# Kernel optimization log

Measured on AMD Instinct MI355X. Metric: run time of the kernel, lower is better.

The kernel has to match this reference:

```python
import jax, jax.numpy as jnp
import numpy as np

N_GRAPHS = 64

def setup_inputs() -> dict:
    key = jax.random.key(0)
    ks = jax.random.split(key, 8)
    N, E, H = 50000, 600000, 128
    x = jax.random.normal(ks[0], (N, 2), dtype=jnp.float32)
    edge_index = jax.random.randint(ks[1], (2, E), 0, N, dtype=jnp.int64)
    batch = jnp.sort(jax.random.randint(ks[2], (N,), 0, N_GRAPHS, dtype=jnp.int64))
    s = 0.1  # keep tanh out of saturation
    return {
        'x': x,
        'edge_index': edge_index,
        'batch': batch,
        'W1': jax.random.normal(ks[3], (2, H), dtype=jnp.float32) * s,
        'b1': jnp.zeros((H,), jnp.float32),
        'W2': jax.random.normal(ks[4], (H, H), dtype=jnp.float32) * s,
        'b2': jnp.zeros((H,), jnp.float32),
        'W3': jax.random.normal(ks[5], (H, H), dtype=jnp.float32) * s,
        'b3': jnp.zeros((H,), jnp.float32),
        'Wo': jax.random.normal(ks[6], (2 * H, 41), dtype=jnp.float32) * s,
        'bo': jnp.zeros((41,), jnp.float32),
    }

def reference(x, edge_index, batch, W1, b1, W2, b2, W3, b3, Wo, bo):
    N = x.shape[0]
    src, dst = edge_index[0], edge_index[1]
    # GCN symmetric normalization with self loops: deg = in-degree + 1
    ones_e = jnp.ones(src.shape[0], dtype=x.dtype)
    deg = jax.ops.segment_sum(ones_e, dst, num_segments=N) + 1.0
    dinv = jax.lax.rsqrt(deg)                       # [N]
    edge_norm = (dinv[src] * dinv[dst])[:, None]    # [E,1]
    self_norm = (dinv * dinv)[:, None]              # [N,1]

    def gcn(h, W, b):
        h = h @ W                                   # [N,H] transform first
        agg = jax.ops.segment_sum(h[src] * edge_norm, dst, num_segments=N)
        return agg + h * self_norm + b

    h = jnp.tanh(gcn(x, W1, b1))
    h = jnp.tanh(gcn(h, W2, b2))
    h = jnp.tanh(gcn(h, W3, b3))

    # global max pool + global mean pool over graphs
    cnt = jax.ops.segment_sum(jnp.ones(N, dtype=h.dtype), batch, num_segments=N_GRAPHS)
    mx = jax.ops.segment_max(h, batch, num_segments=N_GRAPHS)
    mx = jnp.where(cnt[:, None] > 0, mx, 0.0)
    mean = jax.ops.segment_sum(h, batch, num_segments=N_GRAPHS) / jnp.maximum(cnt, 1.0)[:, None]
    pooled = jnp.concatenate([mx, mean], axis=1)    # [G, 2H]
    return jnp.tanh(pooled @ Wo + bo)               # [G, 41]
```

## Files before the change

### kernel.cpp

```cpp
#include <hip/hip_runtime.h>
#include <math.h>

#define NGRAPH 64
#define SCAN_BLK 1024
#define COLCAP 6144
#define AXCAP 2560

typedef short short8 __attribute__((ext_vector_type(8)));
typedef float floatx4 __attribute__((ext_vector_type(4)));

__device__ inline unsigned pack_bf16x2(float a, float b) {
    unsigned ua = __float_as_uint(a);
    unsigned ub = __float_as_uint(b);
    ua = (ua + 0x7fffu + ((ua >> 16) & 1u)) >> 16;
    ub = (ub + 0x7fffu + ((ub >> 16) & 1u)) >> 16;
    return ua | (ub << 16);
}
__device__ inline float bf16lo(unsigned u) { return __uint_as_float(u << 16); }
__device__ inline float bf16hi(unsigned u) { return __uint_as_float(u & 0xffff0000u); }

__device__ inline float ftanh(float x) {
    float cx = fminf(fmaxf(x, -9.f), 9.f);
    float e = __expf(2.f * cx);
    return (e - 1.f) * __frcp_rn(e + 1.f);
}

__device__ inline unsigned fkey(float v) {
    unsigned u = __float_as_uint(v);
    return (v >= 0.f) ? (u | 0x80000000u) : ~u;
}


#define TIDX(u) ((size_t)((qb + (unsigned)(u)) * 4u + (unsigned)q))
#define ACC4() do {                                                       \
    uint4 v0 = t4[TIDX(u0)]; uint4 v1 = t4[TIDX(u1)];                     \
    uint4 v2 = t4[TIDX(u2)]; uint4 v3 = t4[TIDX(u3)];                     \
    a[0] += bf16lo(v0.x); a[1] += bf16hi(v0.x);                           \
    a[2] += bf16lo(v0.y); a[3] += bf16hi(v0.y);                           \
    a[4] += bf16lo(v0.z); a[5] += bf16hi(v0.z);                           \
    a[6] += bf16lo(v0.w); a[7] += bf16hi(v0.w);                           \
    a[0] += bf16lo(v1.x); a[1] += bf16hi(v1.x);                           \
    a[2] += bf16lo(v1.y); a[3] += bf16hi(v1.y);                           \
    a[4] += bf16lo(v1.z); a[5] += bf16hi(v1.z);                           \
    a[6] += bf16lo(v1.w); a[7] += bf16hi(v1.w);                           \
    a[0] += bf16lo(v2.x); a[1] += bf16hi(v2.x);                           \
    a[2] += bf16lo(v2.y); a[3] += bf16hi(v2.y);                           \
    a[4] += bf16lo(v2.z); a[5] += bf16hi(v2.z);                           \
    a[6] += bf16lo(v2.w); a[7] += bf16hi(v2.w);                           \
    a[0] += bf16lo(v3.x); a[1] += bf16hi(v3.x);                           \
    a[2] += bf16lo(v3.y); a[3] += bf16hi(v3.y);                           \
    a[4] += bf16lo(v3.z); a[5] += bf16hi(v3.z);                           \
    a[6] += bf16lo(v3.w); a[7] += bf16hi(v3.w);                           \
} while (0)
#define ACC4M() do {                                                      \
    uint4 v0 = t4[TIDX(u0)]; uint4 v1 = t4[TIDX(u1)];                     \
    uint4 v2 = t4[TIDX(u2)]; uint4 v3 = t4[TIDX(u3)];                     \
    a[0] += bf16lo(v0.x); a[1] += bf16hi(v0.x);                           \
    a[2] += bf16lo(v0.y); a[3] += bf16hi(v0.y);                           \
    a[4] += bf16lo(v0.z); a[5] += bf16hi(v0.z);                           \
    a[6] += bf16lo(v0.w); a[7] += bf16hi(v0.w);                           \
    a[0] = fmaf(m1, bf16lo(v1.x), a[0]); a[1] = fmaf(m1, bf16hi(v1.x), a[1]); \
    a[2] = fmaf(m1, bf16lo(v1.y), a[2]); a[3] = fmaf(m1, bf16hi(v1.y), a[3]); \
    a[4] = fmaf(m1, bf16lo(v1.z), a[4]); a[5] = fmaf(m1, bf16hi(v1.z), a[5]); \
    a[6] = fmaf(m1, bf16lo(v1.w), a[6]); a[7] = fmaf(m1, bf16hi(v1.w), a[7]); \
    a[0] = fmaf(m2, bf16lo(v2.x), a[0]); a[1] = fmaf(m2, bf16hi(v2.x), a[1]); \
    a[2] = fmaf(m2, bf16lo(v2.y), a[2]); a[3] = fmaf(m2, bf16hi(v2.y), a[3]); \
    a[4] = fmaf(m2, bf16lo(v2.z), a[4]); a[5] = fmaf(m2, bf16hi(v2.z), a[5]); \
    a[6] = fmaf(m2, bf16lo(v2.w), a[6]); a[7] = fmaf(m2, bf16hi(v2.w), a[7]); \
    a[0] = fmaf(m3, bf16lo(v3.x), a[0]); a[1] = fmaf(m3, bf16hi(v3.x), a[1]); \
    a[2] = fmaf(m3, bf16lo(v3.y), a[2]); a[3] = fmaf(m3, bf16hi(v3.y), a[3]); \
    a[4] = fmaf(m3, bf16lo(v3.z), a[4]); a[5] = fmaf(m3, bf16hi(v3.z), a[5]); \
    a[6] = fmaf(m3, bf16lo(v3.w), a[6]); a[7] = fmaf(m3, bf16hi(v3.w), a[7]); \
} while (0)


__global__ void pack_count(const int* __restrict__ dst, int E, int* __restrict__ cnt,
                           int* __restrict__ rank,
                           const float* __restrict__ W2, const float* __restrict__ W3,
                           unsigned* __restrict__ Wt2, unsigned* __restrict__ Wt3) {
    if (blockIdx.x < 32) {
        int b = blockIdx.x;
        const float* W = (b < 16) ? W2 : W3;
        unsigned* Wt = (b < 16) ? Wt2 : Wt3;
        b &= 15;
        int bk = b & 3, bn = b >> 2;
        __shared__ float s[32][33];
        int tx = threadIdx.x & 31, ty = threadIdx.x >> 5;
#pragma unroll
        for (int r = 0; r < 4; ++r)
            s[r * 8 + ty][tx] = W[(bk * 32 + r * 8 + ty) * 128 + bn * 32 + tx];
        __syncthreads();
        int t16 = threadIdx.x & 15, tn = threadIdx.x >> 4;
#pragma unroll
        for (int pass = 0; pass < 2; ++pass) {
            int nl = pass * 16 + tn;
            unsigned pk = pack_bf16x2(s[2 * t16][nl], s[2 * t16 + 1][nl]);
            Wt[(bn * 32 + nl) * 64 + bk * 16 + t16] = pk;
        }
    } else {
        int e = (blockIdx.x - 32) * blockDim.x + threadIdx.x;
        if (e < E) rank[e] = atomicAdd(&cnt[dst[e]], 1);
    }
}


__global__ __launch_bounds__(SCAN_BLK) void scanA(const int* __restrict__ cnt,
                                                  const float* __restrict__ x,
                                                  int* __restrict__ row_ptr,
                                                  int* __restrict__ bsum,
                                                  float* __restrict__ dinv,
                                                  float2* __restrict__ y,
                                                  const int* __restrict__ batch,
                                                  int* __restrict__ ticket,
                                                  int* __restrict__ goff, int N) {
    __shared__ int sm[SCAN_BLK];
    __shared__ int amLast;
    int i = blockIdx.x * SCAN_BLK + threadIdx.x;
    int v = (i < N) ? cnt[i] : 0;
    if (i < N) {
        float dv = rsqrtf((float)v + 1.0f);
        dinv[i] = dv;
        float2 xv = ((const float2*)x)[i];
        y[i] = make_float2(xv.x * dv, xv.y * dv);
    }
    sm[threadIdx.x] = v;
    __syncthreads();
    for (int off = 1; off < SCAN_BLK; off <<= 1) {
        int t = (threadIdx.x >= (unsigned)off) ? sm[threadIdx.x - off] : 0;
        __syncthreads();
        sm[threadIdx.x] += t;
        __syncthreads();
    }
    if (i < N) row_ptr[i] = sm[threadIdx.x] - v;
    if (threadIdx.x == SCAN_BLK - 1) bsum[blockIdx.x] = sm[SCAN_BLK - 1];
    __syncthreads();
    if (threadIdx.x == 0) {
        __threadfence();
        amLast = (atomicAdd(ticket, 1) == (int)gridDim.x - 1);
    }
    __syncthreads();
    if (!amLast) return;
    int nb = (int)gridDim.x;
    int v2 = (threadIdx.x < (unsigned)nb) ? atomicAdd(&bsum[threadIdx.x], 0) : 0;
    sm[threadIdx.x] = v2;
    __syncthreads();
    for (int off = 1; off < SCAN_BLK; off <<= 1) {
        int t = (threadIdx.x >= (unsigned)off) ? sm[threadIdx.x - off] : 0;
        __syncthreads();
        sm[threadIdx.x] += t;
        __syncthreads();
    }
    if (threadIdx.x < (unsigned)nb) bsum[threadIdx.x] = sm[threadIdx.x] - v2;
    if (threadIdx.x <= NGRAPH) {
        int g = threadIdx.x;
        int lo = 0, hi = N;
        while (lo < hi) {
            int mid = (lo + hi) >> 1;
            if (batch[mid] < g) lo = mid + 1; else hi = mid;
        }
        goff[g] = lo;
    }
}

__global__ void fill_kernel(const int* __restrict__ src, const int* __restrict__ dst, int E,
                            const int* __restrict__ row_ptr, const int* __restrict__ bsum,
                            const int* __restrict__ rank, int* __restrict__ col) {
    int e = blockIdx.x * blockDim.x + threadIdx.x;
    if (e < E) {
        int d = dst[e];
        int p = row_ptr[d] + bsum[d >> 10] + rank[e];
        col[p] = src[e];
    }
}


__global__ __launch_bounds__(256) void agg_x_t1(const float2* __restrict__ y,
                                                const int* __restrict__ row_ptr,
                                                const int* __restrict__ bsum,
                                                const int* __restrict__ col,
                                                const float* __restrict__ dinv,
                                                const float* __restrict__ W1,
                                                const float* __restrict__ b1,
                                                unsigned short* __restrict__ h, int N, int E) {
    __shared__ float4 sW[64];
    __shared__ float4 sb[32];
    __shared__ float2 zs[64];
    __shared__ int scol[AXCAP];
    if (threadIdx.x < 64) sW[threadIdx.x] = ((const float4*)W1)[threadIdx.x];
    if (threadIdx.x >= 64 && threadIdx.x < 96) sb[threadIdx.x - 64] = ((const float4*)b1)[threadIdx.x - 64];

    int firstNode = blockIdx.x * 64;
    int lastNode = min(firstNode + 64, N);
    int sBase = row_ptr[firstNode] + bsum[firstNode >> 10];
    int eEnd = (lastNode < N) ? row_ptr[lastNode] + bsum[lastNode >> 10] : E;
    int range = eEnd - sBase;
    bool inLds = (range <= AXCAP);
    if (inLds) {
        for (int i = threadIdx.x; i < range; i += 256) scol[i] = col[sBase + i];
    }
    __syncthreads();

    int grp = threadIdx.x >> 2;
    int l4 = threadIdx.x & 3;
    int node = firstNode + grp;
    float ax = 0.f, ay = 0.f;
    if (node < N) {
        int s = row_ptr[node] + bsum[node >> 10];
        int e = (node + 1 < N) ? row_ptr[node + 1] + bsum[(node + 1) >> 10] : E;
        int deg = e - s;
        if (inLds) {
            int sl = s - sBase;
            int j = l4;
            for (; j + 4 < deg; j += 8) {
                float2 v0 = y[scol[sl + j]];
                float2 v1 = y[scol[sl + j + 4]];
                ax += v0.x; ay += v0.y;
                ax += v1.x; ay += v1.y;
            }
            if (j < deg) { float2 v = y[scol[sl + j]]; ax += v.x; ay += v.y; }
        } else {
            int j = l4;
            for (; j + 4 < deg; j += 8) {
                float2 v0 = y[col[s + j]];
                float2 v1 = y[col[s + j + 4]];
                ax += v0.x; ay += v0.y;
                ax += v1.x; ay += v1.y;
            }
            if (j < deg) { float2 v = y[col[s + j]]; ax += v.x; ay += v.y; }
        }
    }
    ax += __shfl_xor(ax, 1, 64); ay += __shfl_xor(ay, 1, 64);
    ax += __shfl_xor(ax, 2, 64); ay += __shfl_xor(ay, 2, 64);
    if (l4 == 0 && node < N) {
        float2 self = y[node];
        float dv = dinv[node];
        zs[grp] = make_float2(dv * (ax + self.x), dv * (ay + self.y));
    }
    __syncthreads();

    int q = threadIdx.x & 31;
    int rsub = threadIdx.x >> 5;
    float4 w0 = sW[q];
    float4 w1 = sW[32 + q];
    float4 b = sb[q];
    size_t qoff = (size_t)(q >> 3) * N;
#pragma unroll
    for (int pass = 0; pass < 8; ++pass) {
        int local = pass * 8 + rsub;
        int row = firstNode + local;
        if (row >= N) break;
        float2 z = zs[local];
        float ox = ftanh(fmaf(z.x, w0.x, fmaf(z.y, w1.x, b.x)));
        float oy = ftanh(fmaf(z.x, w0.y, fmaf(z.y, w1.y, b.y)));
        float oz = ftanh(fmaf(z.x, w0.z, fmaf(z.y, w1.z, b.z)));
        float ow = ftanh(fmaf(z.x, w0.w, fmaf(z.y, w1.w, b.w)));
        uint2 pk;
        pk.x = pack_bf16x2(ox, oy);
        pk.y = pack_bf16x2(oz, ow);
        ((uint2*)h)[(qoff + row) * 8 + (q & 7)] = pk;
    }
}


__global__ __launch_bounds__(256) void gemm_mfma(const unsigned short* __restrict__ A,
                                                 const unsigned* __restrict__ Wt,
                                                 const float* __restrict__ dinv,
                                                 unsigned short* __restrict__ t, int N) {
    __shared__ unsigned sW[128 * 68];
    const uint4* Wt4 = (const uint4*)Wt;
    for (int i = threadIdx.x; i < 2048; i += 256) {
        int n = i >> 4, c = i & 15;
        *(uint4*)&sW[n * 68 + c * 4] = Wt4[i];
    }
    __syncthreads();
    int l = threadIdx.x & 63;
    int w = threadIdx.x >> 6;
    int lm = l & 15;
    int q4 = l >> 4;

    floatx4 acc[2][8];
#pragma unroll
    for (int i = 0; i < 2; ++i)
#pragma unroll
        for (int j = 0; j < 8; ++j) acc[i][j] = (floatx4){0.f, 0.f, 0.f, 0.f};

    int rowbase = blockIdx.x * 128 + w * 32;
    int k8 = q4 * 8;
#pragma unroll
    for (int ks = 0; ks < 4; ++ks) {
        short8 a[2];
#pragma unroll
        for (int mt = 0; mt < 2; ++mt) {
            int r = min(rowbase + mt * 16 + lm, N - 1);
            a[mt] = *(const short8*)(A + ((size_t)ks * N + r) * 32 + k8);
        }
#pragma unroll
        for (int nt = 0; nt < 8; ++nt) {
            short8 b = *(const short8*)&sW[(nt * 16 + lm) * 68 + ks * 16 + q4 * 4];
#pragma unroll
            for (int mt = 0; mt < 2; ++mt)
                acc[mt][nt] = __builtin_amdgcn_mfma_f32_16x16x32_bf16(b, a[mt], acc[mt][nt], 0, 0, 0);
        }
    }

#pragma unroll
    for (int mt = 0; mt < 2; ++mt) {
        int gr = rowbase + mt * 16 + lm;
        if (gr < N) {
            float dv = dinv[gr];
#pragma unroll
            for (int nt = 0; nt < 8; ++nt) {
                uint2 pk;
                pk.x = pack_bf16x2(acc[mt][nt][0] * dv, acc[mt][nt][1] * dv);
                pk.y = pack_bf16x2(acc[mt][nt][2] * dv, acc[mt][nt][3] * dv);
                *(uint2*)(t + ((size_t)(nt >> 1) * N + gr) * 32 + (nt & 1) * 16 + q4 * 4) = pk;
            }
        }
    }
}


__global__ __launch_bounds__(1024) void agg_kernel(const unsigned short* __restrict__ t,
                                                   const int* __restrict__ row_ptr,
                                                   const int* __restrict__ bsum,
                                                   const int* __restrict__ col,
                                                   const float* __restrict__ dinv,
                                                   const float* __restrict__ bias,
                                                   unsigned short* __restrict__ out, int N, int E) {
    int nchunk = (N + 255) >> 8;
    int bid = (int)blockIdx.x;
    int r8 = bid & 7;
    int qt = r8 >> 1;
    int c = (bid >> 3) * 2 + (r8 & 1);
    if (c >= nchunk) return;

    __shared__ int scol[COLCAP];
    int firstNode = c * 256;
    int lastNode = min(firstNode + 256, N);
    int sBase = row_ptr[firstNode] + bsum[firstNode >> 10];
    int eEnd = (lastNode < N) ? row_ptr[lastNode] + bsum[lastNode >> 10] : E;
    int range = eEnd - sBase;
    bool inLds = (range <= COLCAP);
    if (inLds) {
        for (int i = threadIdx.x; i < range; i += 1024) scol[i] = col[sBase + i];
    }
    __syncthreads();

    int q = threadIdx.x & 3;
    int node = firstNode + ((int)threadIdx.x >> 2);
    if (node >= N) return;
    const uint4* t4 = (const uint4*)t;
    unsigned qb = (unsigned)qt * (unsigned)N;
    int s = row_ptr[node] + bsum[node >> 10];
    int e = (node + 1 < N) ? row_ptr[node + 1] + bsum[(node + 1) >> 10] : E;
    int deg = e - s;

    float a[8];
    {
        uint4 v = t4[TIDX(node)];
        a[0] = bf16lo(v.x); a[1] = bf16hi(v.x);
        a[2] = bf16lo(v.y); a[3] = bf16hi(v.y);
        a[4] = bf16lo(v.z); a[5] = bf16hi(v.z);
        a[6] = bf16lo(v.w); a[7] = bf16hi(v.w);
    }
    int j = 0;
    if (inLds) {
        int sl = s - sBase;
        for (; j + 4 <= deg; j += 4) {
            int u0 = scol[sl + j], u1 = scol[sl + j + 1];
            int u2 = scol[sl + j + 2], u3 = scol[sl + j + 3];
            ACC4();
        }
        if (j < deg) {
            float m1 = (j + 1 < deg) ? 1.f : 0.f;
            float m2 = (j + 2 < deg) ? 1.f : 0.f;
            float m3 = (j + 3 < deg) ? 1.f : 0.f;
            int u0 = scol[sl + j];
            int u1 = scol[sl + min(j + 1, deg - 1)];
            int u2 = scol[sl + min(j + 2, deg - 1)];
            int u3 = scol[sl + min(j + 3, deg - 1)];
            ACC4M();
        }
    } else {
        for (; j + 4 <= deg; j += 4) {
            int u0 = col[s + j], u1 = col[s + j + 1];
            int u2 = col[s + j + 2], u3 = col[s + j + 3];
            ACC4();
        }
        if (j < deg) {
            float m1 = (j + 1 < deg) ? 1.f : 0.f;
            float m2 = (j + 2 < deg) ? 1.f : 0.f;
            float m3 = (j + 3 < deg) ? 1.f : 0.f;
            int u0 = col[s + j];
            int u1 = col[s + min(j + 1, deg - 1)];
            int u2 = col[s + min(j + 2, deg - 1)];
            int u3 = col[s + min(j + 3, deg - 1)];
            ACC4M();
        }
    }

    float dv = dinv[node];
    const float4* b4 = (const float4*)bias;
    float4 b0 = b4[qt * 8 + q * 2];
    float4 b1 = b4[qt * 8 + q * 2 + 1];
    uint4 pk;
    pk.x = pack_bf16x2(ftanh(fmaf(dv, a[0], b0.x)), ftanh(fmaf(dv, a[1], b0.y)));
    pk.y = pack_bf16x2(ftanh(fmaf(dv, a[2], b0.z)), ftanh(fmaf(dv, a[3], b0.w)));
    pk.z = pack_bf16x2(ftanh(fmaf(dv, a[4], b1.x)), ftanh(fmaf(dv, a[5], b1.y)));
    pk.w = pack_bf16x2(ftanh(fmaf(dv, a[6], b1.z)), ftanh(fmaf(dv, a[7], b1.w)));
    ((uint4*)out)[TIDX(node)] = pk;
}


__global__ __launch_bounds__(1024) void agg3_pool(const unsigned short* __restrict__ t,
                                                  const int* __restrict__ row_ptr,
                                                  const int* __restrict__ bsum,
                                                  const int* __restrict__ col,
                                                  const float* __restrict__ dinv,
                                                  const float* __restrict__ bias,
                                                  const int* __restrict__ batch,
                                                  unsigned* __restrict__ pmax,
                                                  float* __restrict__ psum, int N, int E) {
    int nchunk = (N + 255) >> 8;
    int bid = (int)blockIdx.x;
    int r8 = bid & 7;
    int qt = r8 >> 1;
    int c = (bid >> 3) * 2 + (r8 & 1);
    if (c >= nchunk) return;

    __shared__ unsigned smax[2][32];
    __shared__ float ssum[2][32];
    __shared__ int scol[COLCAP];
    if (threadIdx.x < 64) {
        smax[threadIdx.x >> 5][threadIdx.x & 31] = 0u;
        ssum[threadIdx.x >> 5][threadIdx.x & 31] = 0.f;
    }
    int firstNode = c * 256;
    int lastNode = min(firstNode + 256, N);
    int sBase = row_ptr[firstNode] + bsum[firstNode >> 10];
    int eEnd = (lastNode < N) ? row_ptr[lastNode] + bsum[lastNode >> 10] : E;
    int range = eEnd - sBase;
    bool inLds = (range <= COLCAP);
    if (inLds) {
        for (int i = threadIdx.x; i < range; i += 1024) scol[i] = col[sBase + i];
    }
    __syncthreads();

    int q = threadIdx.x & 3;
    int blockBase = firstNode;
    int node = blockBase + ((int)threadIdx.x >> 2);
    bool valid = node < N;
    int nc = valid ? node : N - 1;
    const uint4* t4 = (const uint4*)t;
    unsigned qb = (unsigned)qt * (unsigned)N;
    int s = row_ptr[nc] + bsum[nc >> 10];
    int e = (nc + 1 < N) ? row_ptr[nc + 1] + bsum[(nc + 1) >> 10] : E;
    int deg = valid ? (e - s) : 0;

    float a[8];
    {
        uint4 v = t4[TIDX(nc)];
        a[0] = bf16lo(v.x); a[1] = bf16hi(v.x);
        a[2] = bf16lo(v.y); a[3] = bf16hi(v.y);
        a[4] = bf16lo(v.z); a[5] = bf16hi(v.z);
        a[6] = bf16lo(v.w); a[7] = bf16hi(v.w);
    }
    int j = 0;
    if (inLds) {
        int sl = s - sBase;
        for (; j + 4 <= deg; j += 4) {
            int u0 = scol[sl + j], u1 = scol[sl + j + 1];
            int u2 = scol[sl + j + 2], u3 = scol[sl + j + 3];
            ACC4();
        }
        if (j < deg) {
            float m1 = (j + 1 < deg) ? 1.f : 0.f;
            float m2 = (j + 2 < deg) ? 1.f : 0.f;
            float m3 = (j + 3 < deg) ? 1.f : 0.f;
            int u0 = scol[sl + j];
            int u1 = scol[sl + min(j + 1, deg - 1)];
            int u2 = scol[sl + min(j + 2, deg - 1)];
            int u3 = scol[sl + min(j + 3, deg - 1)];
            ACC4M();
        }
    } else {
        for (; j + 4 <= deg; j += 4) {
            int u0 = col[s + j], u1 = col[s + j + 1];
            int u2 = col[s + j + 2], u3 = col[s + j + 3];
            ACC4();
        }
        if (j < deg) {
            float m1 = (j + 1 < deg) ? 1.f : 0.f;
            float m2 = (j + 2 < deg) ? 1.f : 0.f;
            float m3 = (j + 3 < deg) ? 1.f : 0.f;
            int u0 = col[s + j];
            int u1 = col[s + min(j + 1, deg - 1)];
            int u2 = col[s + min(j + 2, deg - 1)];
            int u3 = col[s + min(j + 3, deg - 1)];
            ACC4M();
        }
    }

    float dv = dinv[nc];
    const float4* b4 = (const float4*)bias;
    float4 b0 = b4[qt * 8 + q * 2];
    float4 b1 = b4[qt * 8 + q * 2 + 1];
    float o[8];
    o[0] = ftanh(fmaf(dv, a[0], b0.x)); o[1] = ftanh(fmaf(dv, a[1], b0.y));
    o[2] = ftanh(fmaf(dv, a[2], b0.z)); o[3] = ftanh(fmaf(dv, a[3], b0.w));
    o[4] = ftanh(fmaf(dv, a[4], b1.x)); o[5] = ftanh(fmaf(dv, a[5], b1.y));
    o[6] = ftanh(fmaf(dv, a[6], b1.z)); o[7] = ftanh(fmaf(dv, a[7], b1.w));

    int g = batch[nc];
    int g0 = batch[min(blockBase, N - 1)];
    int gl = __shfl(g, 0, 64);
    int gh = __shfl(g, 63, 64);

    if (gl == gh) {
        float m[8], sv[8];
#pragma unroll
        for (int k = 0; k < 8; ++k) {
            m[k] = valid ? o[k] : -3.402823466e+38f;
            sv[k] = valid ? o[k] : 0.f;
        }
#pragma unroll
        for (int st = 4; st < 64; st <<= 1) {
#pragma unroll
            for (int k = 0; k < 8; ++k) {
                m[k] = fmaxf(m[k], __shfl_xor(m[k], st, 64));
                sv[k] += __shfl_xor(sv[k], st, 64);
            }
        }
        if (((threadIdx.x & 63) >> 2) == 0) {
            int seg = gl - g0;
            if (seg < 2) {
#pragma unroll
                for (int k = 0; k < 8; ++k) {
                    atomicMax(&smax[seg][q * 8 + k], fkey(m[k]));
                    atomicAdd(&ssum[seg][q * 8 + k], sv[k]);
                }
            } else {
#pragma unroll
                for (int k = 0; k < 8; ++k) {
                    atomicMax(&pmax[gl * 128 + qt * 32 + q * 8 + k], fkey(m[k]));
                    atomicAdd(&psum[gl * 128 + qt * 32 + q * 8 + k], sv[k]);
                }
            }
        }
    } else {
        if (valid) {
            int seg = g - g0;
            if (seg < 2) {
#pragma unroll
                for (int k = 0; k < 8; ++k) {
                    atomicMax(&smax[seg][q * 8 + k], fkey(o[k]));
                    atomicAdd(&ssum[seg][q * 8 + k], o[k]);
                }
            } else {
#pragma unroll
                for (int k = 0; k < 8; ++k) {
                    atomicMax(&pmax[g * 128 + qt * 32 + q * 8 + k], fkey(o[k]));
                    atomicAdd(&psum[g * 128 + qt * 32 + q * 8 + k], o[k]);
                }
            }
        }
    }
    __syncthreads();
    if (threadIdx.x < 64) {
        int seg = threadIdx.x >> 5, cc = threadIdx.x & 31;
        int g0b = batch[min(blockBase, N - 1)];
        int gg = g0b + seg;
        if (gg < NGRAPH) {
            atomicMax(&pmax[gg * 128 + qt * 32 + cc], smax[seg][cc]);
            atomicAdd(&psum[gg * 128 + qt * 32 + cc], ssum[seg][cc]);
        }
    }
}


__global__ __launch_bounds__(128) void pool_final(const unsigned* __restrict__ pmax,
                                                  const float* __restrict__ psum,
                                                  const int* __restrict__ goff,
                                                  const float* __restrict__ Wo,
                                                  const float* __restrict__ bo,
                                                  float* __restrict__ out) {
    __shared__ float p[256];
    int g = blockIdx.x;
    int j = threadIdx.x;
    int cnt = goff[g + 1] - goff[g];
    unsigned key = pmax[g * 128 + j];
    float mx = (key & 0x80000000u) ? __uint_as_float(key ^ 0x80000000u)
                                   : __uint_as_float(~key);
    p[j] = (cnt > 0) ? mx : 0.f;
    p[128 + j] = psum[g * 128 + j] / fmaxf((float)cnt, 1.f);
    __syncthreads();
    if (j < 41) {
        float acc = bo[j];
        for (int k = 0; k < 256; ++k) acc = fmaf(p[k], Wo[k * 41 + j], acc);
        out[g * 41 + j] = tanhf(acc);
    }
}


extern "C" void kernel_launch(void* const* d_in, const int* in_sizes, int n_in,
                              void* d_out, int out_size, void* d_ws, size_t ws_size,
                              hipStream_t stream) {
    const float* x   = (const float*)d_in[0];
    const int*   ei  = (const int*)d_in[1];
    const int* batch = (const int*)d_in[2];
    const float* W1  = (const float*)d_in[3];
    const float* b1  = (const float*)d_in[4];
    const float* W2  = (const float*)d_in[5];
    const float* b2  = (const float*)d_in[6];
    const float* W3  = (const float*)d_in[7];
    const float* b3  = (const float*)d_in[8];
    const float* Wo  = (const float*)d_in[9];
    const float* bo  = (const float*)d_in[10];
    float* outp = (float*)d_out;

    int N = in_sizes[2];
    int E = in_sizes[1] / 2;
    const int* src = ei;
    const int* dst = ei + E;

    char* p = (char*)d_ws;
    auto alloc = [&](size_t bytes) -> char* {
        char* q = p;
        p += (bytes + 255) & ~(size_t)255;
        return q;
    };
    unsigned short* t   = (unsigned short*)alloc((size_t)N * 128 * 2);
    unsigned short* hb  = (unsigned short*)alloc((size_t)N * 128 * 2);
    float* dinv   = (float*)alloc((size_t)N * 4);
    int*   rowp   = (int*)alloc((size_t)(N + 1) * 4);
    int*   col    = (int*)alloc((size_t)E * 4);
    int*   rank   = (int*)alloc((size_t)E * 4);
    int*   goff   = (int*)alloc(65 * 4);
    float2* y     = (float2*)alloc((size_t)N * 8);
    unsigned* Wt2 = (unsigned*)alloc(128 * 64 * 4);
    unsigned* Wt3 = (unsigned*)alloc(128 * 64 * 4);
    int nscan = (N + SCAN_BLK - 1) / SCAN_BLK;
    int*   bsum   = (int*)alloc((size_t)nscan * 4);
    size_t cntB = ((size_t)N * 4 + 255) & ~(size_t)255;
    char* zbase = alloc(cntB + 256 + NGRAPH * 128 * 4 * 2);
    int*      cnt  = (int*)zbase;
    int*      tick = (int*)(zbase + cntB);
    unsigned* pmax = (unsigned*)(zbase + cntB + 256);
    float*    psum = (float*)(zbase + cntB + 256 + NGRAPH * 128 * 4);

    (void)hipMemsetAsync(zbase, 0, cntB + 256 + NGRAPH * 128 * 4 * 2, stream);

    pack_count<<<32 + (E + 255) / 256, 256, 0, stream>>>(dst, E, cnt, rank, W2, W3, Wt2, Wt3);
    scanA<<<nscan, SCAN_BLK, 0, stream>>>(cnt, x, rowp, bsum, dinv, y, batch, tick, goff, N);
    fill_kernel<<<(E + 255) / 256, 256, 0, stream>>>(src, dst, E, rowp, bsum, rank, col);

    int nchunk = (N + 255) >> 8;
    int nchunkR = (nchunk + 1) & ~1;
    int nblk = nchunkR * 4;

    agg_x_t1<<<(N + 63) / 64, 256, 0, stream>>>(y, rowp, bsum, col, dinv, W1, b1, hb, N, E);
    gemm_mfma<<<(N + 127) / 128, 256, 0, stream>>>(hb, Wt2, dinv, t, N);
    agg_kernel<<<nblk, 1024, 0, stream>>>(t, rowp, bsum, col, dinv, b2, hb, N, E);
    gemm_mfma<<<(N + 127) / 128, 256, 0, stream>>>(hb, Wt3, dinv, t, N);
    agg3_pool<<<nblk, 1024, 0, stream>>>(t, rowp, bsum, col, dinv, b3, batch, pmax, psum, N, E);

    pool_final<<<NGRAPH, 128, 0, stream>>>(pmax, psum, goff, Wo, bo, outp);
}
```

Before: 231.6 us.

## Schedule aggregation nodes by degree-sorted permutation within each graph

Builds a counting-sort permutation of nodes keyed by (graph id, clamped in-degree) during the scan kernel and fill kernel, then has all three aggregation kernels process nodes in that permuted order. Grouping nodes of similar degree in a wavefront is meant to reduce divergence and load imbalance in the per-node edge loops. In exchange it drops the LDS staging of column indices (neighbors are no longer contiguous per block), adds global atomics for the histogram and permutation, a serial 4K-bin scan in the last scan block, and scattered writes and reads through perm.

```diff
diff --git a/kernel.cpp b/kernel.cpp
--- a/kernel.cpp
+++ b/kernel.cpp
@@ -3,8 +3,6 @@
 
 #define NGRAPH 64
 #define SCAN_BLK 1024
-#define COLCAP 6144
-#define AXCAP 2560
 
 typedef short short8 __attribute__((ext_vector_type(8)));
 typedef float floatx4 __attribute__((ext_vector_type(4)));
@@ -112,7 +110,9 @@
                                                   float2* __restrict__ y,
                                                   const int* __restrict__ batch,
                                                   int* __restrict__ ticket,
-                                                  int* __restrict__ goff, int N) {
+                                                  int* __restrict__ goff,
+                                                  int* __restrict__ key,
+                                                  int* __restrict__ khist, int N) {
     __shared__ int sm[SCAN_BLK];
     __shared__ int amLast;
     int i = blockIdx.x * SCAN_BLK + threadIdx.x;
@@ -122,6 +122,9 @@
         dinv[i] = dv;
         float2 xv = ((const float2*)x)[i];
         y[i] = make_float2(xv.x * dv, xv.y * dv);
+        int kb = batch[i] * 64 + min(v, 63);
+        key[i] = kb;
+        atomicAdd(&khist[kb], 1);
     }
     sm[threadIdx.x] = v;
     __syncthreads();
@@ -160,16 +163,45 @@
         }
         goff[g] = lo;
     }
+    __syncthreads();
+    int base = 0;
+    for (int chunk = 0; chunk < 4; ++chunk) {
+        int idx = chunk * SCAN_BLK + threadIdx.x;
+        int val = atomicAdd(&khist[idx], 0);
+        sm[threadIdx.x] = val;
+        __syncthreads();
+        for (int off = 1; off < SCAN_BLK; off <<= 1) {
+            int t = (threadIdx.x >= (unsigned)off) ? sm[threadIdx.x - off] : 0;
+            __syncthreads();
+            sm[threadIdx.x] += t;
+            __syncthreads();
+        }
+        int tot = sm[SCAN_BLK - 1];
+        khist[idx] = sm[threadIdx.x] - val + base;
+        base += tot;
+        __syncthreads();
+    }
 }
 
 __global__ void fill_kernel(const int* __restrict__ src, const int* __restrict__ dst, int E,
                             const int* __restrict__ row_ptr, const int* __restrict__ bsum,
-                            const int* __restrict__ rank, int* __restrict__ col) {
-    int e = blockIdx.x * blockDim.x + threadIdx.x;
-    if (e < E) {
-        int d = dst[e];
-        int p = row_ptr[d] + bsum[d >> 10] + rank[e];
-        col[p] = src[e];
+                            const int* __restrict__ rank, int* __restrict__ col,
+                            const int* __restrict__ key, int* __restrict__ khist,
+                            int* __restrict__ perm, int N, int nPermBlk) {
+    int b = (int)blockIdx.x;
+    if (b < nPermBlk) {
+        int i = b * 256 + (int)threadIdx.x;
+        if (i < N) {
+            int pos = atomicAdd(&khist[key[i]], 1);
+            perm[pos] = i;
+        }
+    } else {
+        int e = (b - nPermBlk) * 256 + (int)threadIdx.x;
+        if (e < E) {
+            int d = dst[e];
+            int p = row_ptr[d] + bsum[d >> 10] + rank[e];
+            col[p] = src[e];
+        }
     }
 }
 
@@ -178,6 +210,7 @@
                                                 const int* __restrict__ row_ptr,
                                                 const int* __restrict__ bsum,
                                                 const int* __restrict__ col,
+                                                const int* __restrict__ perm,
                                                 const float* __restrict__ dinv,
                                                 const float* __restrict__ W1,
                                                 const float* __restrict__ b1,
@@ -185,56 +218,37 @@
     __shared__ float4 sW[64];
     __shared__ float4 sb[32];
     __shared__ float2 zs[64];
-    __shared__ int scol[AXCAP];
+    __shared__ int snode[64];
     if (threadIdx.x < 64) sW[threadIdx.x] = ((const float4*)W1)[threadIdx.x];
     if (threadIdx.x >= 64 && threadIdx.x < 96) sb[threadIdx.x - 64] = ((const float4*)b1)[threadIdx.x - 64];
 
-    int firstNode = blockIdx.x * 64;
-    int lastNode = min(firstNode + 64, N);
-    int sBase = row_ptr[firstNode] + bsum[firstNode >> 10];
-    int eEnd = (lastNode < N) ? row_ptr[lastNode] + bsum[lastNode >> 10] : E;
-    int range = eEnd - sBase;
-    bool inLds = (range <= AXCAP);
-    if (inLds) {
-        for (int i = threadIdx.x; i < range; i += 256) scol[i] = col[sBase + i];
-    }
-    __syncthreads();
-
+    int firstSlot = blockIdx.x * 64;
     int grp = threadIdx.x >> 2;
     int l4 = threadIdx.x & 3;
-    int node = firstNode + grp;
+    int slot = firstSlot + grp;
+    int node = -1;
     float ax = 0.f, ay = 0.f;
-    if (node < N) {
+    if (slot < N) {
+        node = perm[slot];
         int s = row_ptr[node] + bsum[node >> 10];
         int e = (node + 1 < N) ? row_ptr[node + 1] + bsum[(node + 1) >> 10] : E;
         int deg = e - s;
-        if (inLds) {
-            int sl = s - sBase;
-            int j = l4;
-            for (; j + 4 < deg; j += 8) {
-                float2 v0 = y[scol[sl + j]];
-                float2 v1 = y[scol[sl + j + 4]];
-                ax += v0.x; ay += v0.y;
-                ax += v1.x; ay += v1.y;
-            }
-            if (j < deg) { float2 v = y[scol[sl + j]]; ax += v.x; ay += v.y; }
-        } else {
-            int j = l4;
-            for (; j + 4 < deg; j += 8) {
-                float2 v0 = y[col[s + j]];
-                float2 v1 = y[col[s + j + 4]];
-                ax += v0.x; ay += v0.y;
-                ax += v1.x; ay += v1.y;
-            }
-            if (j < deg) { float2 v = y[col[s + j]]; ax += v.x; ay += v.y; }
-        }
+        int j = l4;
+        for (; j + 4 < deg; j += 8) {
+            float2 v0 = y[col[s + j]];
+            float2 v1 = y[col[s + j + 4]];
+            ax += v0.x; ay += v0.y;
+            ax += v1.x; ay += v1.y;
+        }
+        if (j < deg) { float2 v = y[col[s + j]]; ax += v.x; ay += v.y; }
     }
     ax += __shfl_xor(ax, 1, 64); ay += __shfl_xor(ay, 1, 64);
     ax += __shfl_xor(ax, 2, 64); ay += __shfl_xor(ay, 2, 64);
-    if (l4 == 0 && node < N) {
+    if (l4 == 0 && slot < N) {
         float2 self = y[node];
         float dv = dinv[node];
         zs[grp] = make_float2(dv * (ax + self.x), dv * (ay + self.y));
+        snode[grp] = node;
     }
     __syncthreads();
 
@@ -247,9 +261,9 @@
 #pragma unroll
     for (int pass = 0; pass < 8; ++pass) {
         int local = pass * 8 + rsub;
-        int row = firstNode + local;
-        if (row >= N) break;
+        if (firstSlot + local >= N) break;
         float2 z = zs[local];
+        int row = snode[local];
         float ox = ftanh(fmaf(z.x, w0.x, fmaf(z.y, w1.x, b.x)));
         float oy = ftanh(fmaf(z.x, w0.y, fmaf(z.y, w1.y, b.y)));
         float oz = ftanh(fmaf(z.x, w0.z, fmaf(z.y, w1.z, b.z)));
@@ -324,6 +338,7 @@
                                                    const int* __restrict__ row_ptr,
                                                    const int* __restrict__ bsum,
                                                    const int* __restrict__ col,
+                                                   const int* __restrict__ perm,
                                                    const float* __restrict__ dinv,
                                                    const float* __restrict__ bias,
                                                    unsigned short* __restrict__ out, int N, int E) {
@@ -334,21 +349,10 @@
     int c = (bid >> 3) * 2 + (r8 & 1);
     if (c >= nchunk) return;
 
-    __shared__ int scol[COLCAP];
-    int firstNode = c * 256;
-    int lastNode = min(firstNode + 256, N);
-    int sBase = row_ptr[firstNode] + bsum[firstNode >> 10];
-    int eEnd = (lastNode < N) ? row_ptr[lastNode] + bsum[lastNode >> 10] : E;
-    int range = eEnd - sBase;
-    bool inLds = (range <= COLCAP);
-    if (inLds) {
-        for (int i = threadIdx.x; i < range; i += 1024) scol[i] = col[sBase + i];
-    }
-    __syncthreads();
-
     int q = threadIdx.x & 3;
-    int node = firstNode + ((int)threadIdx.x >> 2);
-    if (node >= N) return;
+    int slot = c * 256 + ((int)threadIdx.x >> 2);
+    if (slot >= N) return;
+    int node = perm[slot];
     const uint4* t4 = (const uint4*)t;
     unsigned qb = (unsigned)qt * (unsigned)N;
     int s = row_ptr[node] + bsum[node >> 10];
@@ -364,39 +368,20 @@
         a[6] = bf16lo(v.w); a[7] = bf16hi(v.w);
     }
     int j = 0;
-    if (inLds) {
-        int sl = s - sBase;
-        for (; j + 4 <= deg; j += 4) {
-            int u0 = scol[sl + j], u1 = scol[sl + j + 1];
-            int u2 = scol[sl + j + 2], u3 = scol[sl + j + 3];
-            ACC4();
-        }
-        if (j < deg) {
-            float m1 = (j + 1 < deg) ? 1.f : 0.f;
-            float m2 = (j + 2 < deg) ? 1.f : 0.f;
-            float m3 = (j + 3 < deg) ? 1.f : 0.f;
-            int u0 = scol[sl + j];
-            int u1 = scol[sl + min(j + 1, deg - 1)];
-            int u2 = scol[sl + min(j + 2, deg - 1)];
-            int u3 = scol[sl + min(j + 3, deg - 1)];
-            ACC4M();
-        }
-    } else {
-        for (; j + 4 <= deg; j += 4) {
-            int u0 = col[s + j], u1 = col[s + j + 1];
-            int u2 = col[s + j + 2], u3 = col[s + j + 3];
-            ACC4();
-        }
-        if (j < deg) {
-            float m1 = (j + 1 < deg) ? 1.f : 0.f;
-            float m2 = (j + 2 < deg) ? 1.f : 0.f;
-            float m3 = (j + 3 < deg) ? 1.f : 0.f;
-            int u0 = col[s + j];
-            int u1 = col[s + min(j + 1, deg - 1)];
-            int u2 = col[s + min(j + 2, deg - 1)];
-            int u3 = col[s + min(j + 3, deg - 1)];
-            ACC4M();
-        }
+    for (; j + 4 <= deg; j += 4) {
+        int u0 = col[s + j], u1 = col[s + j + 1];
+        int u2 = col[s + j + 2], u3 = col[s + j + 3];
+        ACC4();
+    }
+    if (j < deg) {
+        float m1 = (j + 1 < deg) ? 1.f : 0.f;
+        float m2 = (j + 2 < deg) ? 1.f : 0.f;
+        float m3 = (j + 3 < deg) ? 1.f : 0.f;
+        int u0 = col[s + j];
+        int u1 = col[s + min(j + 1, deg - 1)];
+        int u2 = col[s + min(j + 2, deg - 1)];
+        int u3 = col[s + min(j + 3, deg - 1)];
+        ACC4M();
     }
 
     float dv = dinv[node];
@@ -416,6 +401,7 @@
                                                   const int* __restrict__ row_ptr,
                                                   const int* __restrict__ bsum,
                                                   const int* __restrict__ col,
+                                                  const int* __restrict__ perm,
                                                   const float* __restrict__ dinv,
                                                   const float* __restrict__ bias,
                                                   const int* __restrict__ batch,
@@ -430,27 +416,17 @@
 
     __shared__ unsigned smax[2][32];
     __shared__ float ssum[2][32];
-    __shared__ int scol[COLCAP];
     if (threadIdx.x < 64) {
         smax[threadIdx.x >> 5][threadIdx.x & 31] = 0u;
         ssum[threadIdx.x >> 5][threadIdx.x & 31] = 0.f;
     }
-    int firstNode = c * 256;
-    int lastNode = min(firstNode + 256, N);
-    int sBase = row_ptr[firstNode] + bsum[firstNode >> 10];
-    int eEnd = (lastNode < N) ? row_ptr[lastNode] + bsum[lastNode >> 10] : E;
-    int range = eEnd - sBase;
-    bool inLds = (range <= COLCAP);
-    if (inLds) {
-        for (int i = threadIdx.x; i < range; i += 1024) scol[i] = col[sBase + i];
-    }
     __syncthreads();
 
     int q = threadIdx.x & 3;
-    int blockBase = firstNode;
-    int node = blockBase + ((int)threadIdx.x >> 2);
-    bool valid = node < N;
-    int nc = valid ? node : N - 1;
+    int blockBase = c * 256;
+    int slot = blockBase + ((int)threadIdx.x >> 2);
+    bool valid = slot < N;
+    int nc = perm[valid ? slot : (N - 1)];
     const uint4* t4 = (const uint4*)t;
     unsigned qb = (unsigned)qt * (unsigned)N;
     int s = row_ptr[nc] + bsum[nc >> 10];
@@ -466,39 +442,20 @@
         a[6] = bf16lo(v.w); a[7] = bf16hi(v.w);
     }
     int j = 0;
-    if (inLds) {
-        int sl = s - sBase;
-        for (; j + 4 <= deg; j += 4) {
-            int u0 = scol[sl + j], u1 = scol[sl + j + 1];
-            int u2 = scol[sl + j + 2], u3 = scol[sl + j + 3];
-            ACC4();
-        }
-        if (j < deg) {
-            float m1 = (j + 1 < deg) ? 1.f : 0.f;
-            float m2 = (j + 2 < deg) ? 1.f : 0.f;
-            float m3 = (j + 3 < deg) ? 1.f : 0.f;
-            int u0 = scol[sl + j];
-            int u1 = scol[sl + min(j + 1, deg - 1)];
-            int u2 = scol[sl + min(j + 2, deg - 1)];
-            int u3 = scol[sl + min(j + 3, deg - 1)];
-            ACC4M();
-        }
-    } else {
-        for (; j + 4 <= deg; j += 4) {
-            int u0 = col[s + j], u1 = col[s + j + 1];
-            int u2 = col[s + j + 2], u3 = col[s + j + 3];
-            ACC4();
-        }
-        if (j < deg) {
-            float m1 = (j + 1 < deg) ? 1.f : 0.f;
-            float m2 = (j + 2 < deg) ? 1.f : 0.f;
-            float m3 = (j + 3 < deg) ? 1.f : 0.f;
-            int u0 = col[s + j];
-            int u1 = col[s + min(j + 1, deg - 1)];
-            int u2 = col[s + min(j + 2, deg - 1)];
-            int u3 = col[s + min(j + 3, deg - 1)];
-            ACC4M();
-        }
+    for (; j + 4 <= deg; j += 4) {
+        int u0 = col[s + j], u1 = col[s + j + 1];
+        int u2 = col[s + j + 2], u3 = col[s + j + 3];
+        ACC4();
+    }
+    if (j < deg) {
+        float m1 = (j + 1 < deg) ? 1.f : 0.f;
+        float m2 = (j + 2 < deg) ? 1.f : 0.f;
+        float m3 = (j + 3 < deg) ? 1.f : 0.f;
+        int u0 = col[s + j];
+        int u1 = col[s + min(j + 1, deg - 1)];
+        int u2 = col[s + min(j + 2, deg - 1)];
+        int u3 = col[s + min(j + 3, deg - 1)];
+        ACC4M();
     }
 
     float dv = dinv[nc];
@@ -512,7 +469,7 @@
     o[6] = ftanh(fmaf(dv, a[6], b1.z)); o[7] = ftanh(fmaf(dv, a[7], b1.w));
 
     int g = batch[nc];
-    int g0 = batch[min(blockBase, N - 1)];
+    int g0 = batch[perm[min(blockBase, N - 1)]];
     int gl = __shfl(g, 0, 64);
     int gh = __shfl(g, 63, 64);
 
@@ -533,7 +490,7 @@
         }
         if (((threadIdx.x & 63) >> 2) == 0) {
             int seg = gl - g0;
-            if (seg < 2) {
+            if (seg >= 0 && seg < 2) {
 #pragma unroll
                 for (int k = 0; k < 8; ++k) {
                     atomicMax(&smax[seg][q * 8 + k], fkey(m[k]));
@@ -550,7 +507,7 @@
     } else {
         if (valid) {
             int seg = g - g0;
-            if (seg < 2) {
+            if (seg >= 0 && seg < 2) {
 #pragma unroll
                 for (int k = 0; k < 8; ++k) {
                     atomicMax(&smax[seg][q * 8 + k], fkey(o[k]));
@@ -568,7 +525,7 @@
     __syncthreads();
     if (threadIdx.x < 64) {
         int seg = threadIdx.x >> 5, cc = threadIdx.x & 31;
-        int g0b = batch[min(blockBase, N - 1)];
+        int g0b = batch[perm[min(blockBase, N - 1)]];
         int gg = g0b + seg;
         if (gg < NGRAPH) {
             atomicMax(&pmax[gg * 128 + qt * 32 + cc], smax[seg][cc]);
@@ -635,6 +592,8 @@
     int*   rowp   = (int*)alloc((size_t)(N + 1) * 4);
     int*   col    = (int*)alloc((size_t)E * 4);
     int*   rank   = (int*)alloc((size_t)E * 4);
+    int*   keyb   = (int*)alloc((size_t)N * 4);
+    int*   perm   = (int*)alloc((size_t)N * 4);
     int*   goff   = (int*)alloc(65 * 4);
     float2* y     = (float2*)alloc((size_t)N * 8);
     unsigned* Wt2 = (unsigned*)alloc(128 * 64 * 4);
@@ -642,27 +601,32 @@
     int nscan = (N + SCAN_BLK - 1) / SCAN_BLK;
     int*   bsum   = (int*)alloc((size_t)nscan * 4);
     size_t cntB = ((size_t)N * 4 + 255) & ~(size_t)255;
-    char* zbase = alloc(cntB + 256 + NGRAPH * 128 * 4 * 2);
-    int*      cnt  = (int*)zbase;
-    int*      tick = (int*)(zbase + cntB);
-    unsigned* pmax = (unsigned*)(zbase + cntB + 256);
-    float*    psum = (float*)(zbase + cntB + 256 + NGRAPH * 128 * 4);
-
-    (void)hipMemsetAsync(zbase, 0, cntB + 256 + NGRAPH * 128 * 4 * 2, stream);
+    size_t poolB = (size_t)NGRAPH * 128 * 4;
+    char* zbase = alloc(cntB + 256 + poolB * 2 + 4096 * 4);
+    int*      cnt   = (int*)zbase;
+    int*      tick  = (int*)(zbase + cntB);
+    unsigned* pmax  = (unsigned*)(zbase + cntB + 256);
+    float*    psum  = (float*)(zbase + cntB + 256 + poolB);
+    int*      khist = (int*)(zbase + cntB + 256 + poolB * 2);
+
+    (void)hipMemsetAsync(zbase, 0, cntB + 256 + poolB * 2 + 4096 * 4, stream);
 
     pack_count<<<32 + (E + 255) / 256, 256, 0, stream>>>(dst, E, cnt, rank, W2, W3, Wt2, Wt3);
-    scanA<<<nscan, SCAN_BLK, 0, stream>>>(cnt, x, rowp, bsum, dinv, y, batch, tick, goff, N);
-    fill_kernel<<<(E + 255) / 256, 256, 0, stream>>>(src, dst, E, rowp, bsum, rank, col);
+    scanA<<<nscan, SCAN_BLK, 0, stream>>>(cnt, x, rowp, bsum, dinv, y, batch, tick, goff,
+                                          keyb, khist, N);
+    int nPermBlk = (N + 255) / 256;
+    fill_kernel<<<nPermBlk + (E + 255) / 256, 256, 0, stream>>>(src, dst, E, rowp, bsum, rank,
+                                                                col, keyb, khist, perm, N, nPermBlk);
 
     int nchunk = (N + 255) >> 8;
     int nchunkR = (nchunk + 1) & ~1;
     int nblk = nchunkR * 4;
 
-    agg_x_t1<<<(N + 63) / 64, 256, 0, stream>>>(y, rowp, bsum, col, dinv, W1, b1, hb, N, E);
+    agg_x_t1<<<(N + 63) / 64, 256, 0, stream>>>(y, rowp, bsum, col, perm, dinv, W1, b1, hb, N, E);
     gemm_mfma<<<(N + 127) / 128, 256, 0, stream>>>(hb, Wt2, dinv, t, N);
-    agg_kernel<<<nblk, 1024, 0, stream>>>(t, rowp, bsum, col, dinv, b2, hb, N, E);
+    agg_kernel<<<nblk, 1024, 0, stream>>>(t, rowp, bsum, col, perm, dinv, b2, hb, N, E);
     gemm_mfma<<<(N + 127) / 128, 256, 0, stream>>>(hb, Wt3, dinv, t, N);
-    agg3_pool<<<nblk, 1024, 0, stream>>>(t, rowp, bsum, col, dinv, b3, batch, pmax, psum, N, E);
+    agg3_pool<<<nblk, 1024, 0, stream>>>(t, rowp, bsum, col, perm, dinv, b3, batch, pmax, psum, N, E);
 
     pool_final<<<NGRAPH, 128, 0, stream>>>(pmax, psum, goff, Wo, bo, outp);
 }
```

Measured after the change: 248.9 us. 7.4% more time.
